# Optimization experiments

Measured on AMD Instinct MI355X. Metric: run time of the kernel, lower is better.

## Reference

```python
import jax, jax.numpy as jnp
import numpy as np

N_NODES = 100000
N_EDGES = 1600000
IN_CH = 128
HID = 128
NUM_CLASSES = 10
NUM_GRAPHS = 128
SLOPE = 0.01  # F.leaky_relu default negative_slope


def _lin_params(key, fan_in, fan_out):
    kw, kb = jax.random.split(key)
    bound = 1.0 / np.sqrt(fan_in)
    W = jax.random.uniform(kw, (fan_in, fan_out), jnp.float32, -bound, bound)
    b = jax.random.uniform(kb, (fan_out,), jnp.float32, -bound, bound)
    return W, b


def setup_inputs() -> dict:
    key = jax.random.key(0)
    ks = jax.random.split(key, 8)
    x = jax.random.normal(ks[0], (N_NODES, IN_CH), jnp.float32)
    edge_index = jax.random.randint(ks[1], (2, N_EDGES), 0, N_NODES, jnp.int64)
    batch = jnp.sort(jax.random.randint(ks[2], (N_NODES,), 0, NUM_GRAPHS, jnp.int64))
    W1, b1 = _lin_params(ks[3], IN_CH, HID)
    W2, b2 = _lin_params(ks[4], HID, HID)
    W3, b3 = _lin_params(ks[5], HID, HID // 2)
    W4, b4 = _lin_params(ks[6], HID // 2, HID // 2)
    W5, b5 = _lin_params(ks[7], HID // 2, NUM_CLASSES)
    return {"x": x, "edge_index": edge_index, "batch": batch,
            "W1": W1, "b1": b1, "W2": W2, "b2": b2,
            "W3": W3, "b3": b3, "W4": W4, "b4": b4, "W5": W5, "b5": b5}


def gcn_conv(x, src, dst, W, b):
    # PyG GCNConv: h = x W; add self-loops; symmetric norm D^-1/2 (A+I) D^-1/2
    h = x @ W  # [N, F]
    n = x.shape[0]
    deg = jnp.zeros((n,), h.dtype).at[dst].add(1.0) + 1.0  # includes self-loop
    dinv = jax.lax.rsqrt(deg)
    norm = dinv[src] * dinv[dst]  # [E]
    agg = jnp.zeros_like(h).at[dst].add(h[src] * norm[:, None])
    agg = agg + h * (dinv * dinv)[:, None]  # self-loop term: 1/deg
    return agg + b


def reference(x, edge_index, batch, W1, b1, W2, b2, W3, b3, W4, b4, W5, b5):
    src, dst = edge_index[0], edge_index[1]
    h = jax.nn.leaky_relu(gcn_conv(x, src, dst, W1, b1), SLOPE)
    h = jax.nn.leaky_relu(gcn_conv(h, src, dst, W2, b2), SLOPE)
    # global mean pool over graphs
    sums = jax.ops.segment_sum(h, batch, num_segments=NUM_GRAPHS)
    cnts = jax.ops.segment_sum(jnp.ones((h.shape[0],), h.dtype), batch,
                               num_segments=NUM_GRAPHS)
    g = sums / jnp.maximum(cnts, 1.0)[:, None]  # [NUM_GRAPHS, HID]
    g = jax.nn.leaky_relu(g @ W3 + b3, SLOPE)
    g = jax.nn.leaky_relu(g @ W4 + b4, SLOPE)
    return g @ W5 + b5
```

## Files before the change

kernel.cpp:

```cpp
#include <hip/hip_runtime.h>
#include <hip/hip_bf16.h>


#define SLOPE 0.01f

__device__ __forceinline__ float lrelu(float x) { return x > 0.f ? x : SLOPE * x; }

__device__ __forceinline__ unsigned short f2bf(float f) {
    union { float f; unsigned u; } v; v.f = f;
    unsigned r = v.u + 0x7fffu + ((v.u >> 16) & 1u);
    return (unsigned short)(r >> 16);
}
__device__ __forceinline__ float bf2f(unsigned short h) {
    union { unsigned u; float f; } v; v.u = ((unsigned)h) << 16;
    return v.f;
}
__device__ __forceinline__ float bf_lo(unsigned x) {
    union { unsigned u; float f; } v; v.u = x << 16; return v.f;
}
__device__ __forceinline__ float bf_hi(unsigned x) {
    union { unsigned u; float f; } v; v.u = x & 0xffff0000u; return v.f;
}
__device__ __forceinline__ unsigned packbf(float lo, float hi) {
    return (unsigned)f2bf(lo) | ((unsigned)f2bf(hi) << 16);
}

typedef __attribute__((ext_vector_type(8))) short bf16x8;
typedef __attribute__((ext_vector_type(4))) float f32x4;
typedef __attribute__((ext_vector_type(2))) float f32x2;

#define LDA 136
#define CAPP 5120
#define MAXBUCK 400

__global__ void k_init(int* __restrict__ zbase, int nz,
                       const float* __restrict__ W1, unsigned short* __restrict__ WT1,
                       const float* __restrict__ W2, unsigned short* __restrict__ WT2) {
    int b = blockIdx.x;
    if (b < 64) {
        int idx = b * 256 + threadIdx.x;
        int k = idx >> 7, n = idx & 127;
        WT1[n * 128 + k] = f2bf(W1[idx]);
    } else if (b < 128) {
        int idx = (b - 64) * 256 + threadIdx.x;
        int k = idx >> 7, n = idx & 127;
        WT2[n * 128 + k] = f2bf(W2[idx]);
    } else {
        int i = (b - 128) * 256 + threadIdx.x;
        if (i < nz) zbase[i] = 0;
    }
}

template<bool IN_BF16, bool SCALE>
__device__ __forceinline__ void gemm_body(const void* __restrict__ Xv,
                                          const unsigned short* __restrict__ WT,
                                          unsigned short* __restrict__ Y, int M,
                                          unsigned short* Bs, int bid,
                                          const float* __restrict__ dinvg) {
    int t = threadIdx.x;
    int row0 = bid * 64;
    int w = t >> 6, l = t & 63;
    int lr = l & 15;
    int ko = (l >> 4) * 8;

    int gr = row0 + w * 16 + lr;
    bool inb = gr < M;
    bf16x8 afr[4];
    if (IN_BF16) {
        const unsigned short* Xrow = (const unsigned short*)Xv + (size_t)gr * 128;
#pragma unroll
        for (int kc = 0; kc < 4; ++kc) {
            if (inb) afr[kc] = *(const bf16x8*)&Xrow[kc * 32 + ko];
            else     afr[kc] = (bf16x8){0, 0, 0, 0, 0, 0, 0, 0};
        }
    } else {
        const float* Xrow = (const float*)Xv + (size_t)gr * 128;
#pragma unroll
        for (int kc = 0; kc < 4; ++kc) {
            if (inb) {
                float4 u0 = *(const float4*)&Xrow[kc * 32 + ko];
                float4 u1 = *(const float4*)&Xrow[kc * 32 + ko + 4];
                union { bf16x8 v; unsigned u[4]; } cv;
                cv.u[0] = packbf(u0.x, u0.y);
                cv.u[1] = packbf(u0.z, u0.w);
                cv.u[2] = packbf(u1.x, u1.y);
                cv.u[3] = packbf(u1.z, u1.w);
                afr[kc] = cv.v;
            } else afr[kc] = (bf16x8){0, 0, 0, 0, 0, 0, 0, 0};
        }
    }

    {
        const uint4* WT4 = (const uint4*)WT;
#pragma unroll
        for (int i = 0; i < 8; ++i) {
            int idx = t + i * 256;
            int n = idx >> 4, c8 = idx & 15;
            *(uint4*)&Bs[n * LDA + c8 * 8] = WT4[idx];
        }
    }
    __syncthreads();

    f32x4 acc[8];
#pragma unroll
    for (int c = 0; c < 8; ++c) acc[c] = (f32x4){0.f, 0.f, 0.f, 0.f};

#pragma unroll
    for (int kc = 0; kc < 4; ++kc) {
        int kb = kc * 32 + ko;
        bf16x8 bfr[8];
#pragma unroll
        for (int ct = 0; ct < 8; ++ct)
            bfr[ct] = *(const bf16x8*)&Bs[(ct * 16 + lr) * LDA + kb];
#pragma unroll
        for (int ct = 0; ct < 8; ++ct)
            acc[ct] = __builtin_amdgcn_mfma_f32_16x16x32_bf16(afr[kc], bfr[ct], acc[ct], 0, 0, 0);
    }

    __syncthreads();
    int qr = (l >> 4) * 4;
#pragma unroll
    for (int i = 0; i < 4; ++i) {
        int r = w * 16 + qr + i;
        float sc = 1.f;
        if (SCALE) {
            int gr2 = row0 + r;
            sc = (gr2 < M) ? dinvg[gr2] : 1.f;
        }
#pragma unroll
        for (int ct = 0; ct < 8; ++ct)
            Bs[r * LDA + ct * 16 + lr] = f2bf(acc[ct][i] * sc);
    }
    __syncthreads();
    {
        uint4* Y4 = (uint4*)Y;
#pragma unroll
        for (int i = 0; i < 4; ++i) {
            int idx = t + i * 256;
            int r = idx >> 4, c8 = idx & 15;
            int g2 = row0 + r;
            if (g2 < M) Y4[(size_t)g2 * 16 + c8] = *(const uint4*)&Bs[r * LDA + c8 * 8];
        }
    }
}

__device__ __forceinline__ void p1_body(const int* __restrict__ src,
                                        const int* __restrict__ dst,
                                        int E, int nb, int* __restrict__ g_cnt,
                                        unsigned* __restrict__ part,
                                        int* hist, int bid) {
    int* base = hist + MAXBUCK;
    int t = threadIdx.x;
    for (int b = t; b < nb; b += 256) hist[b] = 0;
    __syncthreads();
    int e0b = bid * 4096;
#pragma unroll
    for (int j = 0; j < 4; ++j) {
        int e = e0b + j * 1024 + t * 4;
        if (e + 3 < E) {
            int4 d = *(const int4*)&dst[e];
            atomicAdd(&hist[d.x >> 8], 1);
            atomicAdd(&hist[d.y >> 8], 1);
            atomicAdd(&hist[d.z >> 8], 1);
            atomicAdd(&hist[d.w >> 8], 1);
        } else {
            for (int k = e; k < E && k < e + 4; ++k)
                atomicAdd(&hist[dst[k] >> 8], 1);
        }
    }
    __syncthreads();
    for (int b = t; b < nb; b += 256) {
        int c = hist[b];
        base[b] = c ? atomicAdd(&g_cnt[b], c) : 0;
        hist[b] = 0;
    }
    __syncthreads();
#pragma unroll
    for (int j = 0; j < 4; ++j) {
        int e = e0b + j * 1024 + t * 4;
        if (e + 3 < E) {
            int4 d = *(const int4*)&dst[e];
            int4 s = *(const int4*)&src[e];
            int bk, p;
            bk = d.x >> 8; p = base[bk] + atomicAdd(&hist[bk], 1);
            if (p < CAPP) part[(size_t)bk * CAPP + p] = ((unsigned)s.x << 8) | ((unsigned)d.x & 255u);
            bk = d.y >> 8; p = base[bk] + atomicAdd(&hist[bk], 1);
            if (p < CAPP) part[(size_t)bk * CAPP + p] = ((unsigned)s.y << 8) | ((unsigned)d.y & 255u);
            bk = d.z >> 8; p = base[bk] + atomicAdd(&hist[bk], 1);
            if (p < CAPP) part[(size_t)bk * CAPP + p] = ((unsigned)s.z << 8) | ((unsigned)d.z & 255u);
            bk = d.w >> 8; p = base[bk] + atomicAdd(&hist[bk], 1);
            if (p < CAPP) part[(size_t)bk * CAPP + p] = ((unsigned)s.w << 8) | ((unsigned)d.w & 255u);
        } else {
            for (int k = e; k < E && k < e + 4; ++k) {
                int bk = dst[k] >> 8;
                int p = base[bk] + atomicAdd(&hist[bk], 1);
                if (p < CAPP) part[(size_t)bk * CAPP + p] = ((unsigned)src[k] << 8) | ((unsigned)dst[k] & 255u);
            }
        }
    }
}

__global__ __launch_bounds__(256) void k_p1_gemm1(
    const int* __restrict__ src, const int* __restrict__ dst, int E, int nb,
    int* __restrict__ g_cnt, unsigned* __restrict__ part, int nbP1,
    const float* __restrict__ X, const unsigned short* __restrict__ WT,
    unsigned short* __restrict__ Y, int M) {
    __shared__ __align__(16) unsigned short Bs[128 * LDA];
    int b = blockIdx.x;
    if (b < nbP1) p1_body(src, dst, E, nb, g_cnt, part, (int*)Bs, b);
    else gemm_body<false, false>((const void*)X, WT, Y, M, Bs, b - nbP1, nullptr);
}

__global__ __launch_bounds__(256) void k_p2(const unsigned* __restrict__ part,
                                            const int* __restrict__ g_cnt,
                                            int* __restrict__ csr,
                                            int2* __restrict__ rpz,
                                            float* __restrict__ dinvg,
                                            unsigned short* __restrict__ H, int N) {
    __shared__ int cnt[256];
    __shared__ int sc[256];
    __shared__ float dvl[256];
    int b = blockIdx.x, t = threadIdx.x;
    int nbase = b << 8;
    int nn = N - nbase; if (nn > 256) nn = 256;

    cnt[t] = 0;
    __syncthreads();

    int Eb = g_cnt[b]; if (Eb > CAPP) Eb = CAPP;
    const unsigned* pp = part + (size_t)b * CAPP;
    for (int i = t; i < Eb; i += 256)
        atomicAdd(&cnt[pp[i] & 255u], 1);
    __syncthreads();

    int v = cnt[t];
    sc[t] = v;
    __syncthreads();
    for (int off = 1; off < 256; off <<= 1) {
        int add = (t >= off) ? sc[t - off] : 0;
        __syncthreads();
        sc[t] += add;
        __syncthreads();
    }
    int excl = sc[t] - v;

    float di = rsqrtf((float)v + 1.0f);
    if (t < nn) {
        rpz[nbase + t] = make_int2(b * CAPP + excl, b * CAPP + excl + v);
        dinvg[nbase + t] = di;
    }
    dvl[t] = di;
    cnt[t] = excl;
    __syncthreads();

    for (int i = t; i < Eb; i += 256) {
        unsigned pv = pp[i];
        int lcl = pv & 255u;
        int p = atomicAdd(&cnt[lcl], 1);
        csr[(size_t)b * CAPP + p] = (int)(pv >> 8);
    }

    uint4* H4 = (uint4*)H;
    int tot = nn * 16;
    for (int i = t; i < tot; i += 256) {
        int r = i >> 4, c = i & 15;
        float d = dvl[r];
        uint4 hv = H4[(size_t)(nbase + r) * 16 + c];
        uint4 o;
        o.x = packbf(bf_lo(hv.x) * d, bf_hi(hv.x) * d);
        o.y = packbf(bf_lo(hv.y) * d, bf_hi(hv.y) * d);
        o.z = packbf(bf_lo(hv.z) * d, bf_hi(hv.z) * d);
        o.w = packbf(bf_lo(hv.w) * d, bf_hi(hv.w) * d);
        H4[(size_t)(nbase + r) * 16 + c] = o;
    }
}

__global__ __launch_bounds__(256) void k_gemm2(
    const void* __restrict__ Xv, const unsigned short* __restrict__ WT,
    unsigned short* __restrict__ Y, int M, const float* __restrict__ dinvg) {
    __shared__ __align__(16) unsigned short Bs[128 * LDA];
    gemm_body<true, true>(Xv, WT, Y, M, Bs, blockIdx.x, dinvg);
}

__device__ __forceinline__ void acc8(f32x2& S0, f32x2& S1, f32x2& S2, f32x2& S3,
                                     uint4 hv) {
    f32x2 t;
    t.x = bf_lo(hv.x); t.y = bf_hi(hv.x); S0 += t;
    t.x = bf_lo(hv.y); t.y = bf_hi(hv.y); S1 += t;
    t.x = bf_lo(hv.z); t.y = bf_hi(hv.z); S2 += t;
    t.x = bf_lo(hv.w); t.y = bf_hi(hv.w); S3 += t;
}

__global__ __launch_bounds__(256) void k_agg7(const unsigned short* __restrict__ H,
                                              const int* __restrict__ csr,
                                              const int2* __restrict__ rpz,
                                              const float* __restrict__ dinvg,
                                              const float* __restrict__ bias,
                                              unsigned short* __restrict__ OUT, int N) {
    int t = threadIdx.x;
    int grp = t >> 4, cl = t & 15;
    int u = blockIdx.x * 16 + grp;
    if (u >= N) return;
    const uint4* H4 = (const uint4*)H;

    int2 rz = rpz[u];
    int e0 = rz.x, e1 = rz.y;
    uint4 hs = H4[(size_t)u * 16 + cl];
    float du = dinvg[u];

    f32x2 A0 = {0.f, 0.f}, A1 = {0.f, 0.f}, A2 = {0.f, 0.f}, A3 = {0.f, 0.f};
    f32x2 B0 = {0.f, 0.f}, B1 = {0.f, 0.f}, B2 = {0.f, 0.f}, B3 = {0.f, 0.f};

    int e = e0;
    while (e < e1) {
        int nn = e1 - e; if (nn > 16) nn = 16;
        int ci = (cl < nn) ? csr[e + cl] : 0;
        int j = 0;
        for (; j + 4 <= nn; j += 4) {
            int i0 = __shfl(ci, j,     16);
            int i1 = __shfl(ci, j + 1, 16);
            int i2 = __shfl(ci, j + 2, 16);
            int i3 = __shfl(ci, j + 3, 16);
            uint4 hA = H4[(size_t)i0 * 16 + cl];
            uint4 hB = H4[(size_t)i1 * 16 + cl];
            uint4 hC = H4[(size_t)i2 * 16 + cl];
            uint4 hD = H4[(size_t)i3 * 16 + cl];
            acc8(A0, A1, A2, A3, hA);
            acc8(B0, B1, B2, B3, hB);
            acc8(A0, A1, A2, A3, hC);
            acc8(B0, B1, B2, B3, hD);
        }
        for (; j < nn; ++j) {
            int i0 = __shfl(ci, j, 16);
            uint4 hA = H4[(size_t)i0 * 16 + cl];
            acc8(A0, A1, A2, A3, hA);
        }
        e += nn;
    }

    acc8(A0, A1, A2, A3, hs);
    A0 += B0; A1 += B1; A2 += B2; A3 += B3;
    float a0 = A0.x, a1 = A0.y, a2 = A1.x, a3 = A1.y;
    float a4 = A2.x, a5 = A2.y, a6 = A3.x, a7 = A3.y;

    float4 c0 = *(const float4*)&bias[cl * 8];
    float4 c1 = *(const float4*)&bias[cl * 8 + 4];
    uint4 o;
    o.x = packbf(lrelu(a0 * du + c0.x), lrelu(a1 * du + c0.y));
    o.y = packbf(lrelu(a2 * du + c0.z), lrelu(a3 * du + c0.w));
    o.z = packbf(lrelu(a4 * du + c1.x), lrelu(a5 * du + c1.y));
    o.w = packbf(lrelu(a6 * du + c1.z), lrelu(a7 * du + c1.w));
    ((uint4*)OUT)[(size_t)u * 16 + cl] = o;
}

#define PCH 128
__global__ __launch_bounds__(256) void k_pool3(const unsigned short* __restrict__ H,
                                               const int* __restrict__ batch,
                                               float* __restrict__ Gsum,
                                               int* __restrict__ Gcnt, int N) {
    int t = threadIdx.x;
    int st = t >> 6, c2 = t & 63;
    int n0 = blockIdx.x * PCH + st * (PCH / 4);
    int n1 = n0 + (PCH / 4); if (n1 > N) n1 = N;
    if (n0 >= N) return;
    float a0 = 0.f, a1 = 0.f;
    int cur = batch[n0], runstart = n0;
    for (int n = n0; n < n1; ++n) {
        int g = batch[n];
        if (g != cur) {
            atomicAdd(&Gsum[cur * 128 + c2 * 2], a0);
            atomicAdd(&Gsum[cur * 128 + c2 * 2 + 1], a1);
            if (c2 == 0) atomicAdd(&Gcnt[cur], n - runstart);
            a0 = a1 = 0.f; cur = g; runstart = n;
        }
        unsigned hv = *(const unsigned*)&H[(size_t)n * 128 + c2 * 2];
        a0 += bf_lo(hv); a1 += bf_hi(hv);
    }
    atomicAdd(&Gsum[cur * 128 + c2 * 2], a0);
    atomicAdd(&Gsum[cur * 128 + c2 * 2 + 1], a1);
    if (c2 == 0) atomicAdd(&Gcnt[cur], n1 - runstart);
}

__global__ __launch_bounds__(64) void k_mlp(const float* __restrict__ Gsum,
                                            const int* __restrict__ Gcnt,
                                            const float* __restrict__ W3, const float* __restrict__ b3,
                                            const float* __restrict__ W4, const float* __restrict__ b4,
                                            const float* __restrict__ W5, const float* __restrict__ b5,
                                            float* __restrict__ OUT) {
    __shared__ float row[128];
    __shared__ float t1[64];
    __shared__ float t2[64];
    int g = blockIdx.x, t = threadIdx.x;
    float inv = 1.0f / fmaxf((float)Gcnt[g], 1.0f);
    row[t]      = Gsum[g * 128 + t] * inv;
    row[t + 64] = Gsum[g * 128 + t + 64] * inv;
    __syncthreads();
    float acc = b3[t];
    for (int k = 0; k < 128; ++k) acc += row[k] * W3[k * 64 + t];
    t1[t] = lrelu(acc);
    __syncthreads();
    acc = b4[t];
    for (int k = 0; k < 64; ++k) acc += t1[k] * W4[k * 64 + t];
    t2[t] = lrelu(acc);
    __syncthreads();
    if (t < 10) {
        acc = b5[t];
        for (int k = 0; k < 64; ++k) acc += t2[k] * W5[k * 10 + t];
        OUT[g * 10 + t] = acc;
    }
}


extern "C" void kernel_launch(void* const* d_in, const int* in_sizes, int n_in,
                              void* d_out, int out_size, void* d_ws, size_t ws_size,
                              hipStream_t stream) {
    const float* x    = (const float*)d_in[0];
    const int*   ei   = (const int*)d_in[1];
    const int*   batch= (const int*)d_in[2];
    const float* W1   = (const float*)d_in[3];
    const float* b1   = (const float*)d_in[4];
    const float* W2   = (const float*)d_in[5];
    const float* b2   = (const float*)d_in[6];
    const float* W3   = (const float*)d_in[7];
    const float* b3   = (const float*)d_in[8];
    const float* W4   = (const float*)d_in[9];
    const float* b4   = (const float*)d_in[10];
    const float* W5   = (const float*)d_in[11];
    const float* b5   = (const float*)d_in[12];
    float* out = (float*)d_out;

    const int N = in_sizes[2];
    const int E = in_sizes[1] / 2;
    const int NG = 128;

    const int* src = ei;
    const int* dst = ei + E;

    char* w = (char*)d_ws;
    unsigned short* bufA = (unsigned short*)w; w += (size_t)N * 128 * 2;
    unsigned short* bufB = (unsigned short*)w; w += (size_t)N * 128 * 2;
    int*   g_cnt = (int*)w;   w += 512 * 4;
    float* gsum  = (float*)w; w += (size_t)NG * 128 * 4;
    int*   gcnt  = (int*)w;   w += (size_t)NG * 4;
    float* dinv  = (float*)w; w += (size_t)N * 4;
    int2*  rpz   = (int2*)w;  w += (size_t)N * 8;
    unsigned* part = (unsigned*)w; w += (size_t)MAXBUCK * CAPP * 4;
    int*   csr   = (int*)w;   w += (size_t)MAXBUCK * CAPP * 4;
    unsigned short* WT1 = (unsigned short*)w; w += 128 * 128 * 2;
    unsigned short* WT2 = (unsigned short*)w; w += 128 * 128 * 2;
    (void)ws_size; (void)n_in; (void)out_size;

    int nbB  = (N + 255) >> 8;
    int nbP1 = (E + 4095) / 4096;
    int nbG  = (N + 63) / 64;
    int nZero = 512 + NG * 128 + NG;
    int nbZ  = (nZero + 255) / 256;

    k_init<<<128 + nbZ, 256, 0, stream>>>(g_cnt, nZero, W1, WT1, W2, WT2);
    k_p1_gemm1<<<nbP1 + nbG, 256, 0, stream>>>(src, dst, E, nbB, g_cnt, part,
                                               nbP1, x, WT1, bufA, N);
    k_p2<<<nbB, 256, 0, stream>>>(part, g_cnt, csr, rpz, dinv, bufA, N);

    int nbA = (N + 15) / 16;

    k_agg7<<<nbA, 256, 0, stream>>>(bufA, csr, rpz, dinv, b1, bufB, N);
    k_gemm2<<<nbG, 256, 0, stream>>>(bufB, WT2, bufA, N, dinv);
    k_agg7<<<nbA, 256, 0, stream>>>(bufA, csr, rpz, dinv, b2, bufB, N);

    int nbP = (N + PCH - 1) / PCH;
    k_pool3<<<nbP, 256, 0, stream>>>(bufB, batch, gsum, gcnt, N);
    k_mlp<<<NG, 64, 0, stream>>>(gsum, gcnt, W3, b3, W4, b4, W5, b5, out);
}
```

Baseline: 332.4 us.

## Use nontemporal loads/stores and per-graph segment pooling via binary-searched starts

Streaming global loads and stores in the edge partition, GEMM, aggregation and pooling kernels become nontemporal, so single-use data is meant to pollute the caches less. Pooling becomes one block per graph. Segment starts come from a binary search over the sorted batch array, computed in the init kernel. This replaces atomic run-length accumulation and removes the need to zero gsum and gcnt. The cost is that pooling now runs on only 128 blocks, which may underuse the GPU, and nontemporal hints could hurt reuse of H rows that aggregation gathers again.

```diff
diff --git a/kernel.cpp b/kernel.cpp
--- a/kernel.cpp
+++ b/kernel.cpp
@@ -11,10 +11,6 @@
     unsigned r = v.u + 0x7fffu + ((v.u >> 16) & 1u);
     return (unsigned short)(r >> 16);
 }
-__device__ __forceinline__ float bf2f(unsigned short h) {
-    union { unsigned u; float f; } v; v.u = ((unsigned)h) << 16;
-    return v.f;
-}
 __device__ __forceinline__ float bf_lo(unsigned x) {
     union { unsigned u; float f; } v; v.u = x << 16; return v.f;
 }
@@ -28,6 +24,30 @@
 typedef __attribute__((ext_vector_type(8))) short bf16x8;
 typedef __attribute__((ext_vector_type(4))) float f32x4;
 typedef __attribute__((ext_vector_type(2))) float f32x2;
+typedef __attribute__((ext_vector_type(4))) unsigned u32x4;
+typedef __attribute__((ext_vector_type(4))) int i32x4;
+typedef __attribute__((ext_vector_type(2))) int i32x2;
+
+__device__ __forceinline__ uint4 nt_load_u4(const void* p) {
+    u32x4 v = __builtin_nontemporal_load((const u32x4*)p);
+    return make_uint4(v.x, v.y, v.z, v.w);
+}
+__device__ __forceinline__ void nt_store_u4(void* p, uint4 q) {
+    u32x4 v = {q.x, q.y, q.z, q.w};
+    __builtin_nontemporal_store(v, (u32x4*)p);
+}
+__device__ __forceinline__ int4 nt_load_i4(const void* p) {
+    i32x4 v = __builtin_nontemporal_load((const i32x4*)p);
+    return make_int4(v.x, v.y, v.z, v.w);
+}
+__device__ __forceinline__ int2 nt_load_i2(const void* p) {
+    i32x2 v = __builtin_nontemporal_load((const i32x2*)p);
+    return make_int2(v.x, v.y);
+}
+__device__ __forceinline__ float4 nt_load_f4(const void* p) {
+    f32x4 v = __builtin_nontemporal_load((const f32x4*)p);
+    return make_float4(v.x, v.y, v.z, v.w);
+}
 
 #define LDA 136
 #define CAPP 5120
@@ -35,7 +55,9 @@
 
 __global__ void k_init(int* __restrict__ zbase, int nz,
                        const float* __restrict__ W1, unsigned short* __restrict__ WT1,
-                       const float* __restrict__ W2, unsigned short* __restrict__ WT2) {
+                       const float* __restrict__ W2, unsigned short* __restrict__ WT2,
+                       const int* __restrict__ batch, int* __restrict__ gstart,
+                       int N, int NG) {
     int b = blockIdx.x;
     if (b < 64) {
         int idx = b * 256 + threadIdx.x;
@@ -45,8 +67,15 @@
         int idx = (b - 64) * 256 + threadIdx.x;
         int k = idx >> 7, n = idx & 127;
         WT2[n * 128 + k] = f2bf(W2[idx]);
+    } else if (b == 128) {
+        int g = threadIdx.x;
+        if (g <= NG) {
+            int lo = 0, hi = N;
+            while (lo < hi) { int mid = (lo + hi) >> 1; if (batch[mid] < g) lo = mid + 1; else hi = mid; }
+            gstart[g] = lo;
+        }
     } else {
-        int i = (b - 128) * 256 + threadIdx.x;
+        int i = (b - 129) * 256 + threadIdx.x;
         if (i < nz) zbase[i] = 0;
     }
 }
@@ -70,7 +99,7 @@
         const unsigned short* Xrow = (const unsigned short*)Xv + (size_t)gr * 128;
 #pragma unroll
         for (int kc = 0; kc < 4; ++kc) {
-            if (inb) afr[kc] = *(const bf16x8*)&Xrow[kc * 32 + ko];
+            if (inb) afr[kc] = __builtin_nontemporal_load((const bf16x8*)&Xrow[kc * 32 + ko]);
             else     afr[kc] = (bf16x8){0, 0, 0, 0, 0, 0, 0, 0};
         }
     } else {
@@ -78,8 +107,8 @@
 #pragma unroll
         for (int kc = 0; kc < 4; ++kc) {
             if (inb) {
-                float4 u0 = *(const float4*)&Xrow[kc * 32 + ko];
-                float4 u1 = *(const float4*)&Xrow[kc * 32 + ko + 4];
+                float4 u0 = nt_load_f4(&Xrow[kc * 32 + ko]);
+                float4 u1 = nt_load_f4(&Xrow[kc * 32 + ko + 4]);
                 union { bf16x8 v; unsigned u[4]; } cv;
                 cv.u[0] = packbf(u0.x, u0.y);
                 cv.u[1] = packbf(u0.z, u0.w);
@@ -139,7 +168,7 @@
             int idx = t + i * 256;
             int r = idx >> 4, c8 = idx & 15;
             int g2 = row0 + r;
-            if (g2 < M) Y4[(size_t)g2 * 16 + c8] = *(const uint4*)&Bs[r * LDA + c8 * 8];
+            if (g2 < M) nt_store_u4(&Y4[(size_t)g2 * 16 + c8], *(const uint4*)&Bs[r * LDA + c8 * 8]);
         }
     }
 }
@@ -158,7 +187,7 @@
     for (int j = 0; j < 4; ++j) {
         int e = e0b + j * 1024 + t * 4;
         if (e + 3 < E) {
-            int4 d = *(const int4*)&dst[e];
+            int4 d = nt_load_i4(&dst[e]);
             atomicAdd(&hist[d.x >> 8], 1);
             atomicAdd(&hist[d.y >> 8], 1);
             atomicAdd(&hist[d.z >> 8], 1);
@@ -179,17 +208,17 @@
     for (int j = 0; j < 4; ++j) {
         int e = e0b + j * 1024 + t * 4;
         if (e + 3 < E) {
-            int4 d = *(const int4*)&dst[e];
-            int4 s = *(const int4*)&src[e];
+            int4 d = nt_load_i4(&dst[e]);
+            int4 s = nt_load_i4(&src[e]);
             int bk, p;
             bk = d.x >> 8; p = base[bk] + atomicAdd(&hist[bk], 1);
-            if (p < CAPP) part[(size_t)bk * CAPP + p] = ((unsigned)s.x << 8) | ((unsigned)d.x & 255u);
+            if (p < CAPP) __builtin_nontemporal_store(((unsigned)s.x << 8) | ((unsigned)d.x & 255u), &part[(size_t)bk * CAPP + p]);
             bk = d.y >> 8; p = base[bk] + atomicAdd(&hist[bk], 1);
-            if (p < CAPP) part[(size_t)bk * CAPP + p] = ((unsigned)s.y << 8) | ((unsigned)d.y & 255u);
+            if (p < CAPP) __builtin_nontemporal_store(((unsigned)s.y << 8) | ((unsigned)d.y & 255u), &part[(size_t)bk * CAPP + p]);
             bk = d.z >> 8; p = base[bk] + atomicAdd(&hist[bk], 1);
-            if (p < CAPP) part[(size_t)bk * CAPP + p] = ((unsigned)s.z << 8) | ((unsigned)d.z & 255u);
+            if (p < CAPP) __builtin_nontemporal_store(((unsigned)s.z << 8) | ((unsigned)d.z & 255u), &part[(size_t)bk * CAPP + p]);
             bk = d.w >> 8; p = base[bk] + atomicAdd(&hist[bk], 1);
-            if (p < CAPP) part[(size_t)bk * CAPP + p] = ((unsigned)s.w << 8) | ((unsigned)d.w & 255u);
+            if (p < CAPP) __builtin_nontemporal_store(((unsigned)s.w << 8) | ((unsigned)d.w & 255u), &part[(size_t)bk * CAPP + p]);
         } else {
             for (int k = e; k < E && k < e + 4; ++k) {
                 int bk = dst[k] >> 8;
@@ -230,7 +259,7 @@
     int Eb = g_cnt[b]; if (Eb > CAPP) Eb = CAPP;
     const unsigned* pp = part + (size_t)b * CAPP;
     for (int i = t; i < Eb; i += 256)
-        atomicAdd(&cnt[pp[i] & 255u], 1);
+        atomicAdd(&cnt[__builtin_nontemporal_load(&pp[i]) & 255u], 1);
     __syncthreads();
 
     int v = cnt[t];
@@ -254,10 +283,10 @@
     __syncthreads();
 
     for (int i = t; i < Eb; i += 256) {
-        unsigned pv = pp[i];
+        unsigned pv = __builtin_nontemporal_load(&pp[i]);
         int lcl = pv & 255u;
         int p = atomicAdd(&cnt[lcl], 1);
-        csr[(size_t)b * CAPP + p] = (int)(pv >> 8);
+        __builtin_nontemporal_store((int)(pv >> 8), &csr[(size_t)b * CAPP + p]);
     }
 
     uint4* H4 = (uint4*)H;
@@ -303,7 +332,7 @@
     if (u >= N) return;
     const uint4* H4 = (const uint4*)H;
 
-    int2 rz = rpz[u];
+    int2 rz = nt_load_i2(&rpz[u]);
     int e0 = rz.x, e1 = rz.y;
     uint4 hs = H4[(size_t)u * 16 + cl];
     float du = dinvg[u];
@@ -314,7 +343,7 @@
     int e = e0;
     while (e < e1) {
         int nn = e1 - e; if (nn > 16) nn = 16;
-        int ci = (cl < nn) ? csr[e + cl] : 0;
+        int ci = (cl < nn) ? __builtin_nontemporal_load(&csr[e + cl]) : 0;
         int j = 0;
         for (; j + 4 <= nn; j += 4) {
             int i0 = __shfl(ci, j,     16);
@@ -350,39 +379,29 @@
     o.y = packbf(lrelu(a2 * du + c0.z), lrelu(a3 * du + c0.w));
     o.z = packbf(lrelu(a4 * du + c1.x), lrelu(a5 * du + c1.y));
     o.w = packbf(lrelu(a6 * du + c1.z), lrelu(a7 * du + c1.w));
-    ((uint4*)OUT)[(size_t)u * 16 + cl] = o;
-}
-
-#define PCH 128
-__global__ __launch_bounds__(256) void k_pool3(const unsigned short* __restrict__ H,
-                                               const int* __restrict__ batch,
-                                               float* __restrict__ Gsum,
-                                               int* __restrict__ Gcnt, int N) {
-    int t = threadIdx.x;
+    nt_store_u4(&((uint4*)OUT)[(size_t)u * 16 + cl], o);
+}
+
+__global__ __launch_bounds__(256) void k_pool4(const unsigned short* __restrict__ H,
+                                               const int* __restrict__ gstart,
+                                               float* __restrict__ Gsum) {
+    __shared__ float red[4][128];
+    int g = blockIdx.x, t = threadIdx.x;
     int st = t >> 6, c2 = t & 63;
-    int n0 = blockIdx.x * PCH + st * (PCH / 4);
-    int n1 = n0 + (PCH / 4); if (n1 > N) n1 = N;
-    if (n0 >= N) return;
+    int gs = gstart[g], ge = gstart[g + 1];
     float a0 = 0.f, a1 = 0.f;
-    int cur = batch[n0], runstart = n0;
-    for (int n = n0; n < n1; ++n) {
-        int g = batch[n];
-        if (g != cur) {
-            atomicAdd(&Gsum[cur * 128 + c2 * 2], a0);
-            atomicAdd(&Gsum[cur * 128 + c2 * 2 + 1], a1);
-            if (c2 == 0) atomicAdd(&Gcnt[cur], n - runstart);
-            a0 = a1 = 0.f; cur = g; runstart = n;
-        }
-        unsigned hv = *(const unsigned*)&H[(size_t)n * 128 + c2 * 2];
+    for (int n = gs + st; n < ge; n += 4) {
+        unsigned hv = __builtin_nontemporal_load((const unsigned*)&H[(size_t)n * 128 + c2 * 2]);
         a0 += bf_lo(hv); a1 += bf_hi(hv);
     }
-    atomicAdd(&Gsum[cur * 128 + c2 * 2], a0);
-    atomicAdd(&Gsum[cur * 128 + c2 * 2 + 1], a1);
-    if (c2 == 0) atomicAdd(&Gcnt[cur], n1 - runstart);
+    red[st][c2 * 2] = a0; red[st][c2 * 2 + 1] = a1;
+    __syncthreads();
+    if (t < 128)
+        Gsum[g * 128 + t] = red[0][t] + red[1][t] + red[2][t] + red[3][t];
 }
 
 __global__ __launch_bounds__(64) void k_mlp(const float* __restrict__ Gsum,
-                                            const int* __restrict__ Gcnt,
+                                            const int* __restrict__ gstart,
                                             const float* __restrict__ W3, const float* __restrict__ b3,
                                             const float* __restrict__ W4, const float* __restrict__ b4,
                                             const float* __restrict__ W5, const float* __restrict__ b5,
@@ -391,7 +410,7 @@
     __shared__ float t1[64];
     __shared__ float t2[64];
     int g = blockIdx.x, t = threadIdx.x;
-    float inv = 1.0f / fmaxf((float)Gcnt[g], 1.0f);
+    float inv = 1.0f / fmaxf((float)(gstart[g + 1] - gstart[g]), 1.0f);
     row[t]      = Gsum[g * 128 + t] * inv;
     row[t + 64] = Gsum[g * 128 + t + 64] * inv;
     __syncthreads();
@@ -441,7 +460,7 @@
     unsigned short* bufB = (unsigned short*)w; w += (size_t)N * 128 * 2;
     int*   g_cnt = (int*)w;   w += 512 * 4;
     float* gsum  = (float*)w; w += (size_t)NG * 128 * 4;
-    int*   gcnt  = (int*)w;   w += (size_t)NG * 4;
+    int*   gstart= (int*)w;   w += 512 * 4;
     float* dinv  = (float*)w; w += (size_t)N * 4;
     int2*  rpz   = (int2*)w;  w += (size_t)N * 8;
     unsigned* part = (unsigned*)w; w += (size_t)MAXBUCK * CAPP * 4;
@@ -453,10 +472,11 @@
     int nbB  = (N + 255) >> 8;
     int nbP1 = (E + 4095) / 4096;
     int nbG  = (N + 63) / 64;
-    int nZero = 512 + NG * 128 + NG;
+    int nZero = 512;
     int nbZ  = (nZero + 255) / 256;
 
-    k_init<<<128 + nbZ, 256, 0, stream>>>(g_cnt, nZero, W1, WT1, W2, WT2);
+    k_init<<<129 + nbZ, 256, 0, stream>>>(g_cnt, nZero, W1, WT1, W2, WT2,
+                                          batch, gstart, N, NG);
     k_p1_gemm1<<<nbP1 + nbG, 256, 0, stream>>>(src, dst, E, nbB, g_cnt, part,
                                                nbP1, x, WT1, bufA, N);
     k_p2<<<nbB, 256, 0, stream>>>(part, g_cnt, csr, rpz, dinv, bufA, N);
@@ -467,7 +487,6 @@
     k_gemm2<<<nbG, 256, 0, stream>>>(bufB, WT2, bufA, N, dinv);
     k_agg7<<<nbA, 256, 0, stream>>>(bufA, csr, rpz, dinv, b2, bufB, N);
 
-    int nbP = (N + PCH - 1) / PCH;
-    k_pool3<<<nbP, 256, 0, stream>>>(bufB, batch, gsum, gcnt, N);
-    k_mlp<<<NG, 64, 0, stream>>>(gsum, gcnt, W3, b3, W4, b4, W5, b5, out);
-}
+    k_pool4<<<NG, 256, 0, stream>>>(bufB, gstart, gsum);
+    k_mlp<<<NG, 64, 0, stream>>>(gsum, gstart, W3, b3, W4, b4, W5, b5, out);
+}
```

New measurement: 469.8 us. +41.3%, slower.

## Slice node features into 8 channel-blocks so each aggregation block gathers a narrow slice

Applied to the files above, without the earlier changes.

Node feature buffers are stored as 8 slices of 16 channels ([slice][node][16]), and the aggregation kernel assigns one slice per block, with two threads per node handling 32 bytes each. The aim is to shrink the per-slice working set (N*32 bytes) so random neighbour gathers hit L2/cache better than 256-byte full-row gathers spread over the whole table. GEMM loads and stores, the dinv rescale, pooling and the MLP channel mapping are all rewritten for the new layout. Separately, per-graph node counts now come from a binary search over the sorted batch array instead of atomic counts in pooling. The cost is that each edge index is read 8 times and each gather uses narrower 32-byte segments.

```diff
diff --git a/kernel.cpp b/kernel.cpp
--- a/kernel.cpp
+++ b/kernel.cpp
@@ -11,10 +11,6 @@
     unsigned r = v.u + 0x7fffu + ((v.u >> 16) & 1u);
     return (unsigned short)(r >> 16);
 }
-__device__ __forceinline__ float bf2f(unsigned short h) {
-    union { unsigned u; float f; } v; v.u = ((unsigned)h) << 16;
-    return v.f;
-}
 __device__ __forceinline__ float bf_lo(unsigned x) {
     union { unsigned u; float f; } v; v.u = x << 16; return v.f;
 }
@@ -33,9 +29,12 @@
 #define CAPP 5120
 #define MAXBUCK 400
 
+
 __global__ void k_init(int* __restrict__ zbase, int nz,
                        const float* __restrict__ W1, unsigned short* __restrict__ WT1,
-                       const float* __restrict__ W2, unsigned short* __restrict__ WT2) {
+                       const float* __restrict__ W2, unsigned short* __restrict__ WT2,
+                       const int* __restrict__ batch, int* __restrict__ gstart,
+                       int N, int NG) {
     int b = blockIdx.x;
     if (b < 64) {
         int idx = b * 256 + threadIdx.x;
@@ -45,8 +44,15 @@
         int idx = (b - 64) * 256 + threadIdx.x;
         int k = idx >> 7, n = idx & 127;
         WT2[n * 128 + k] = f2bf(W2[idx]);
+    } else if (b == 128) {
+        int g = threadIdx.x;
+        if (g <= NG) {
+            int lo = 0, hi = N;
+            while (lo < hi) { int mid = (lo + hi) >> 1; if (batch[mid] < g) lo = mid + 1; else hi = mid; }
+            gstart[g] = lo;
+        }
     } else {
-        int i = (b - 128) * 256 + threadIdx.x;
+        int i = (b - 129) * 256 + threadIdx.x;
         if (i < nz) zbase[i] = 0;
     }
 }
@@ -67,10 +73,11 @@
     bool inb = gr < M;
     bf16x8 afr[4];
     if (IN_BF16) {
-        const unsigned short* Xrow = (const unsigned short*)Xv + (size_t)gr * 128;
+        const unsigned short* Hsb = (const unsigned short*)Xv;
 #pragma unroll
         for (int kc = 0; kc < 4; ++kc) {
-            if (inb) afr[kc] = *(const bf16x8*)&Xrow[kc * 32 + ko];
+            int c0 = kc * 32 + ko;
+            if (inb) afr[kc] = *(const bf16x8*)&Hsb[((size_t)(c0 >> 4) * M + gr) * 16 + (c0 & 15)];
             else     afr[kc] = (bf16x8){0, 0, 0, 0, 0, 0, 0, 0};
         }
     } else {
@@ -139,7 +146,8 @@
             int idx = t + i * 256;
             int r = idx >> 4, c8 = idx & 15;
             int g2 = row0 + r;
-            if (g2 < M) Y4[(size_t)g2 * 16 + c8] = *(const uint4*)&Bs[r * LDA + c8 * 8];
+            if (g2 < M)
+                Y4[((size_t)(c8 >> 1) * M + g2) * 2 + (c8 & 1)] = *(const uint4*)&Bs[r * LDA + c8 * 8];
         }
     }
 }
@@ -263,15 +271,16 @@
     uint4* H4 = (uint4*)H;
     int tot = nn * 16;
     for (int i = t; i < tot; i += 256) {
-        int r = i >> 4, c = i & 15;
+        int r = i >> 4, q = i & 15;
         float d = dvl[r];
-        uint4 hv = H4[(size_t)(nbase + r) * 16 + c];
+        size_t idx = ((size_t)(q >> 1) * N + nbase + r) * 2 + (q & 1);
+        uint4 hv = H4[idx];
         uint4 o;
         o.x = packbf(bf_lo(hv.x) * d, bf_hi(hv.x) * d);
         o.y = packbf(bf_lo(hv.y) * d, bf_hi(hv.y) * d);
         o.z = packbf(bf_lo(hv.z) * d, bf_hi(hv.z) * d);
         o.w = packbf(bf_lo(hv.w) * d, bf_hi(hv.w) * d);
-        H4[(size_t)(nbase + r) * 16 + c] = o;
+        H4[idx] = o;
     }
 }
 
@@ -291,78 +300,76 @@
     t.x = bf_lo(hv.w); t.y = bf_hi(hv.w); S3 += t;
 }
 
-__global__ __launch_bounds__(256) void k_agg7(const unsigned short* __restrict__ H,
+__global__ __launch_bounds__(256) void k_agg8(const unsigned short* __restrict__ Hs,
                                               const int* __restrict__ csr,
                                               const int2* __restrict__ rpz,
                                               const float* __restrict__ dinvg,
                                               const float* __restrict__ bias,
-                                              unsigned short* __restrict__ OUT, int N) {
+                                              unsigned short* __restrict__ OUTs, int N) {
+    int b = blockIdx.x;
+    int s = b & 7;
+    int nb = b >> 3;
     int t = threadIdx.x;
-    int grp = t >> 4, cl = t & 15;
-    int u = blockIdx.x * 16 + grp;
+    int pair = t >> 1, half = t & 1;
+    int u = nb * 128 + pair;
     if (u >= N) return;
-    const uint4* H4 = (const uint4*)H;
+    const uint4* H4 = (const uint4*)Hs + (size_t)s * N * 2;
 
     int2 rz = rpz[u];
-    int e0 = rz.x, e1 = rz.y;
-    uint4 hs = H4[(size_t)u * 16 + cl];
     float du = dinvg[u];
+    uint4 hsv = H4[(size_t)u * 2 + half];
 
     f32x2 A0 = {0.f, 0.f}, A1 = {0.f, 0.f}, A2 = {0.f, 0.f}, A3 = {0.f, 0.f};
     f32x2 B0 = {0.f, 0.f}, B1 = {0.f, 0.f}, B2 = {0.f, 0.f}, B3 = {0.f, 0.f};
-
-    int e = e0;
+    const uint4 z4 = make_uint4(0, 0, 0, 0);
+
+    int e = rz.x, e1 = rz.y;
     while (e < e1) {
-        int nn = e1 - e; if (nn > 16) nn = 16;
-        int ci = (cl < nn) ? csr[e + cl] : 0;
-        int j = 0;
-        for (; j + 4 <= nn; j += 4) {
-            int i0 = __shfl(ci, j,     16);
-            int i1 = __shfl(ci, j + 1, 16);
-            int i2 = __shfl(ci, j + 2, 16);
-            int i3 = __shfl(ci, j + 3, 16);
-            uint4 hA = H4[(size_t)i0 * 16 + cl];
-            uint4 hB = H4[(size_t)i1 * 16 + cl];
-            uint4 hC = H4[(size_t)i2 * 16 + cl];
-            uint4 hD = H4[(size_t)i3 * 16 + cl];
-            acc8(A0, A1, A2, A3, hA);
-            acc8(B0, B1, B2, B3, hB);
-            acc8(A0, A1, A2, A3, hC);
-            acc8(B0, B1, B2, B3, hD);
-        }
-        for (; j < nn; ++j) {
-            int i0 = __shfl(ci, j, 16);
-            uint4 hA = H4[(size_t)i0 * 16 + cl];
-            acc8(A0, A1, A2, A3, hA);
-        }
+        int nn = e1 - e; if (nn > 4) nn = 4;
+        int cA = (e + half < e1)     ? csr[e + half]     : 0;
+        int cB = (e + 2 + half < e1) ? csr[e + 2 + half] : 0;
+        int i0 = __shfl(cA, 0, 2);
+        int i1 = __shfl(cA, 1, 2);
+        int i2 = __shfl(cB, 0, 2);
+        int i3 = __shfl(cB, 1, 2);
+        uint4 h0 =            H4[(size_t)i0 * 2 + half];
+        uint4 h1 = (nn > 1) ? H4[(size_t)i1 * 2 + half] : z4;
+        uint4 h2 = (nn > 2) ? H4[(size_t)i2 * 2 + half] : z4;
+        uint4 h3 = (nn > 3) ? H4[(size_t)i3 * 2 + half] : z4;
+        acc8(A0, A1, A2, A3, h0);
+        acc8(B0, B1, B2, B3, h1);
+        acc8(A0, A1, A2, A3, h2);
+        acc8(B0, B1, B2, B3, h3);
         e += nn;
     }
 
-    acc8(A0, A1, A2, A3, hs);
     A0 += B0; A1 += B1; A2 += B2; A3 += B3;
+    acc8(A0, A1, A2, A3, hsv);
     float a0 = A0.x, a1 = A0.y, a2 = A1.x, a3 = A1.y;
     float a4 = A2.x, a5 = A2.y, a6 = A3.x, a7 = A3.y;
 
-    float4 c0 = *(const float4*)&bias[cl * 8];
-    float4 c1 = *(const float4*)&bias[cl * 8 + 4];
+    const float* bs = bias + s * 16 + half * 8;
+    float4 c0 = *(const float4*)bs;
+    float4 c1 = *(const float4*)(bs + 4);
     uint4 o;
     o.x = packbf(lrelu(a0 * du + c0.x), lrelu(a1 * du + c0.y));
     o.y = packbf(lrelu(a2 * du + c0.z), lrelu(a3 * du + c0.w));
     o.z = packbf(lrelu(a4 * du + c1.x), lrelu(a5 * du + c1.y));
     o.w = packbf(lrelu(a6 * du + c1.z), lrelu(a7 * du + c1.w));
-    ((uint4*)OUT)[(size_t)u * 16 + cl] = o;
+    ((uint4*)OUTs)[((size_t)s * N + u) * 2 + half] = o;
 }
 
 #define PCH 128
-__global__ __launch_bounds__(256) void k_pool3(const unsigned short* __restrict__ H,
+__global__ __launch_bounds__(256) void k_pool5(const unsigned short* __restrict__ H,
                                                const int* __restrict__ batch,
-                                               float* __restrict__ Gsum,
-                                               int* __restrict__ Gcnt, int N) {
+                                               float* __restrict__ Gsum, int N) {
     int t = threadIdx.x;
     int st = t >> 6, c2 = t & 63;
     int n0 = blockIdx.x * PCH + st * (PCH / 4);
     int n1 = n0 + (PCH / 4); if (n1 > N) n1 = N;
     if (n0 >= N) return;
+    size_t sb = (size_t)(c2 >> 3) * N;
+    int off = (c2 & 7) * 2;
     float a0 = 0.f, a1 = 0.f;
     int cur = batch[n0], runstart = n0;
     for (int n = n0; n < n1; ++n) {
@@ -370,19 +377,18 @@
         if (g != cur) {
             atomicAdd(&Gsum[cur * 128 + c2 * 2], a0);
             atomicAdd(&Gsum[cur * 128 + c2 * 2 + 1], a1);
-            if (c2 == 0) atomicAdd(&Gcnt[cur], n - runstart);
             a0 = a1 = 0.f; cur = g; runstart = n;
         }
-        unsigned hv = *(const unsigned*)&H[(size_t)n * 128 + c2 * 2];
+        unsigned hv = *(const unsigned*)&H[(sb + n) * 16 + off];
         a0 += bf_lo(hv); a1 += bf_hi(hv);
     }
     atomicAdd(&Gsum[cur * 128 + c2 * 2], a0);
     atomicAdd(&Gsum[cur * 128 + c2 * 2 + 1], a1);
-    if (c2 == 0) atomicAdd(&Gcnt[cur], n1 - runstart);
+    (void)runstart;
 }
 
 __global__ __launch_bounds__(64) void k_mlp(const float* __restrict__ Gsum,
-                                            const int* __restrict__ Gcnt,
+                                            const int* __restrict__ gstart,
                                             const float* __restrict__ W3, const float* __restrict__ b3,
                                             const float* __restrict__ W4, const float* __restrict__ b4,
                                             const float* __restrict__ W5, const float* __restrict__ b5,
@@ -391,9 +397,13 @@
     __shared__ float t1[64];
     __shared__ float t2[64];
     int g = blockIdx.x, t = threadIdx.x;
-    float inv = 1.0f / fmaxf((float)Gcnt[g], 1.0f);
-    row[t]      = Gsum[g * 128 + t] * inv;
-    row[t + 64] = Gsum[g * 128 + t + 64] * inv;
+    float inv = 1.0f / fmaxf((float)(gstart[g + 1] - gstart[g]), 1.0f);
+    int c2 = t >> 1, lohi = t & 1;
+    int gch = ((c2 >> 3) << 4) + ((c2 & 7) << 1) + lohi;
+    row[gch] = Gsum[g * 128 + t] * inv;
+    c2 = (t + 64) >> 1; lohi = (t + 64) & 1;
+    gch = ((c2 >> 3) << 4) + ((c2 & 7) << 1) + lohi;
+    row[gch] = Gsum[g * 128 + t + 64] * inv;
     __syncthreads();
     float acc = b3[t];
     for (int k = 0; k < 128; ++k) acc += row[k] * W3[k * 64 + t];
@@ -441,7 +451,7 @@
     unsigned short* bufB = (unsigned short*)w; w += (size_t)N * 128 * 2;
     int*   g_cnt = (int*)w;   w += 512 * 4;
     float* gsum  = (float*)w; w += (size_t)NG * 128 * 4;
-    int*   gcnt  = (int*)w;   w += (size_t)NG * 4;
+    int*   gstart= (int*)w;   w += 512 * 4;
     float* dinv  = (float*)w; w += (size_t)N * 4;
     int2*  rpz   = (int2*)w;  w += (size_t)N * 8;
     unsigned* part = (unsigned*)w; w += (size_t)MAXBUCK * CAPP * 4;
@@ -453,21 +463,22 @@
     int nbB  = (N + 255) >> 8;
     int nbP1 = (E + 4095) / 4096;
     int nbG  = (N + 63) / 64;
-    int nZero = 512 + NG * 128 + NG;
+    int nZero = 512 + NG * 128;
     int nbZ  = (nZero + 255) / 256;
 
-    k_init<<<128 + nbZ, 256, 0, stream>>>(g_cnt, nZero, W1, WT1, W2, WT2);
+    k_init<<<129 + nbZ, 256, 0, stream>>>(g_cnt, nZero, W1, WT1, W2, WT2,
+                                          batch, gstart, N, NG);
     k_p1_gemm1<<<nbP1 + nbG, 256, 0, stream>>>(src, dst, E, nbB, g_cnt, part,
                                                nbP1, x, WT1, bufA, N);
     k_p2<<<nbB, 256, 0, stream>>>(part, g_cnt, csr, rpz, dinv, bufA, N);
 
-    int nbA = (N + 15) / 16;
-
-    k_agg7<<<nbA, 256, 0, stream>>>(bufA, csr, rpz, dinv, b1, bufB, N);
+    int nbA = ((N + 127) / 128) * 8;
+
+    k_agg8<<<nbA, 256, 0, stream>>>(bufA, csr, rpz, dinv, b1, bufB, N);
     k_gemm2<<<nbG, 256, 0, stream>>>(bufB, WT2, bufA, N, dinv);
-    k_agg7<<<nbA, 256, 0, stream>>>(bufA, csr, rpz, dinv, b2, bufB, N);
+    k_agg8<<<nbA, 256, 0, stream>>>(bufA, csr, rpz, dinv, b2, bufB, N);
 
     int nbP = (N + PCH - 1) / PCH;
-    k_pool3<<<nbP, 256, 0, stream>>>(bufB, batch, gsum, gcnt, N);
-    k_mlp<<<NG, 64, 0, stream>>>(gsum, gcnt, W3, b3, W4, b4, W5, b5, out);
-}
+    k_pool5<<<nbP, 256, 0, stream>>>(bufB, batch, gsum, N);
+    k_mlp<<<NG, 64, 0, stream>>>(gsum, gstart, W3, b3, W4, b4, W5, b5, out);
+}
```

Result: slower. 498.2 us (+49.9%).

## Fuse layer-1 aggregation with layer-2 GEMM and derive graph counts via binary search

Applied to the files above, without the earlier changes.

Layer-1 neighbor aggregation is now computed straight into shared memory and fed to the MFMA GEMM for layer 2 in the same kernel, so the intermediate activation no longer makes a global-memory round trip and one launch is removed. Per-graph node counts are now derived once from a binary search over the sorted batch array in the init kernel, which removes the count atomics from the pooling kernel. The fused kernel handles 64 rows per block, so there are fewer, heavier blocks for the gather phase, and the B operand is read straight from global memory rather than staged in LDS. The count shortcut depends on batch being sorted.

```diff
diff --git a/kernel.cpp b/kernel.cpp
--- a/kernel.cpp
+++ b/kernel.cpp
@@ -11,10 +11,6 @@
     unsigned r = v.u + 0x7fffu + ((v.u >> 16) & 1u);
     return (unsigned short)(r >> 16);
 }
-__device__ __forceinline__ float bf2f(unsigned short h) {
-    union { unsigned u; float f; } v; v.u = ((unsigned)h) << 16;
-    return v.f;
-}
 __device__ __forceinline__ float bf_lo(unsigned x) {
     union { unsigned u; float f; } v; v.u = x << 16; return v.f;
 }
@@ -35,7 +31,9 @@
 
 __global__ void k_init(int* __restrict__ zbase, int nz,
                        const float* __restrict__ W1, unsigned short* __restrict__ WT1,
-                       const float* __restrict__ W2, unsigned short* __restrict__ WT2) {
+                       const float* __restrict__ W2, unsigned short* __restrict__ WT2,
+                       const int* __restrict__ batch, int* __restrict__ gstart,
+                       int N, int NG) {
     int b = blockIdx.x;
     if (b < 64) {
         int idx = b * 256 + threadIdx.x;
@@ -45,8 +43,15 @@
         int idx = (b - 64) * 256 + threadIdx.x;
         int k = idx >> 7, n = idx & 127;
         WT2[n * 128 + k] = f2bf(W2[idx]);
+    } else if (b == 128) {
+        int g = threadIdx.x;
+        if (g <= NG) {
+            int lo = 0, hi = N;
+            while (lo < hi) { int mid = (lo + hi) >> 1; if (batch[mid] < g) lo = mid + 1; else hi = mid; }
+            gstart[g] = lo;
+        }
     } else {
-        int i = (b - 128) * 256 + threadIdx.x;
+        int i = (b - 129) * 256 + threadIdx.x;
         if (i < nz) zbase[i] = 0;
     }
 }
@@ -275,13 +280,6 @@
     }
 }
 
-__global__ __launch_bounds__(256) void k_gemm2(
-    const void* __restrict__ Xv, const unsigned short* __restrict__ WT,
-    unsigned short* __restrict__ Y, int M, const float* __restrict__ dinvg) {
-    __shared__ __align__(16) unsigned short Bs[128 * LDA];
-    gemm_body<true, true>(Xv, WT, Y, M, Bs, blockIdx.x, dinvg);
-}
-
 __device__ __forceinline__ void acc8(f32x2& S0, f32x2& S1, f32x2& S2, f32x2& S3,
                                      uint4 hv) {
     f32x2 t;
@@ -291,23 +289,11 @@
     t.x = bf_lo(hv.w); t.y = bf_hi(hv.w); S3 += t;
 }
 
-__global__ __launch_bounds__(256) void k_agg7(const unsigned short* __restrict__ H,
-                                              const int* __restrict__ csr,
-                                              const int2* __restrict__ rpz,
-                                              const float* __restrict__ dinvg,
-                                              const float* __restrict__ bias,
-                                              unsigned short* __restrict__ OUT, int N) {
-    int t = threadIdx.x;
-    int grp = t >> 4, cl = t & 15;
-    int u = blockIdx.x * 16 + grp;
-    if (u >= N) return;
-    const uint4* H4 = (const uint4*)H;
-
-    int2 rz = rpz[u];
-    int e0 = rz.x, e1 = rz.y;
+__device__ __forceinline__ uint4 agg_node(const uint4* __restrict__ H4,
+                                          const int* __restrict__ csr,
+                                          int e0, int e1, int u, float du,
+                                          const float* __restrict__ bias, int cl) {
     uint4 hs = H4[(size_t)u * 16 + cl];
-    float du = dinvg[u];
-
     f32x2 A0 = {0.f, 0.f}, A1 = {0.f, 0.f}, A2 = {0.f, 0.f}, A3 = {0.f, 0.f};
     f32x2 B0 = {0.f, 0.f}, B1 = {0.f, 0.f}, B2 = {0.f, 0.f}, B3 = {0.f, 0.f};
 
@@ -350,39 +336,124 @@
     o.y = packbf(lrelu(a2 * du + c0.z), lrelu(a3 * du + c0.w));
     o.z = packbf(lrelu(a4 * du + c1.x), lrelu(a5 * du + c1.y));
     o.w = packbf(lrelu(a6 * du + c1.z), lrelu(a7 * du + c1.w));
+    return o;
+}
+
+__global__ __launch_bounds__(256) void k_aggemm(
+    const unsigned short* __restrict__ H,
+    const int* __restrict__ csr, const int2* __restrict__ rpz,
+    const float* __restrict__ dinvg, const float* __restrict__ bias,
+    const unsigned short* __restrict__ WT,
+    unsigned short* __restrict__ Y, int M) {
+    __shared__ __align__(16) unsigned short As[64 * LDA];
+    int t = threadIdx.x;
+    int row0 = blockIdx.x * 64;
+    int grp = t >> 4, cl = t & 15;
+    const uint4* H4 = (const uint4*)H;
+
+#pragma unroll
+    for (int rd = 0; rd < 4; ++rd) {
+        int r = rd * 16 + grp;
+        int u = row0 + r;
+        uint4 o = make_uint4(0, 0, 0, 0);
+        if (u < M) {
+            int2 rz = rpz[u];
+            float du = dinvg[u];
+            o = agg_node(H4, csr, rz.x, rz.y, u, du, bias, cl);
+        }
+        *(uint4*)&As[r * LDA + cl * 8] = o;
+    }
+    __syncthreads();
+
+    int w = t >> 6, l = t & 63;
+    int lr = l & 15;
+    int ko = (l >> 4) * 8;
+
+    f32x4 acc[8];
+#pragma unroll
+    for (int c = 0; c < 8; ++c) acc[c] = (f32x4){0.f, 0.f, 0.f, 0.f};
+
+#pragma unroll
+    for (int kc = 0; kc < 4; ++kc) {
+        int kb = kc * 32 + ko;
+        bf16x8 afr = *(const bf16x8*)&As[(w * 16 + lr) * LDA + kb];
+        bf16x8 bfr[8];
+#pragma unroll
+        for (int ct = 0; ct < 8; ++ct)
+            bfr[ct] = *(const bf16x8*)&WT[(size_t)(ct * 16 + lr) * 128 + kb];
+#pragma unroll
+        for (int ct = 0; ct < 8; ++ct)
+            acc[ct] = __builtin_amdgcn_mfma_f32_16x16x32_bf16(afr, bfr[ct], acc[ct], 0, 0, 0);
+    }
+
+    __syncthreads();
+    int qr = (l >> 4) * 4;
+#pragma unroll
+    for (int i = 0; i < 4; ++i) {
+        int r = w * 16 + qr + i;
+        int gr2 = row0 + r;
+        float sc = (gr2 < M) ? dinvg[gr2] : 1.f;
+#pragma unroll
+        for (int ct = 0; ct < 8; ++ct)
+            As[r * LDA + ct * 16 + lr] = f2bf(acc[ct][i] * sc);
+    }
+    __syncthreads();
+    {
+        uint4* Y4 = (uint4*)Y;
+#pragma unroll
+        for (int i = 0; i < 4; ++i) {
+            int idx = t + i * 256;
+            int r = idx >> 4, c8 = idx & 15;
+            int g2 = row0 + r;
+            if (g2 < M) Y4[(size_t)g2 * 16 + c8] = *(const uint4*)&As[r * LDA + c8 * 8];
+        }
+    }
+}
+
+__global__ __launch_bounds__(256) void k_agg7(const unsigned short* __restrict__ H,
+                                              const int* __restrict__ csr,
+                                              const int2* __restrict__ rpz,
+                                              const float* __restrict__ dinvg,
+                                              const float* __restrict__ bias,
+                                              unsigned short* __restrict__ OUT, int N) {
+    int t = threadIdx.x;
+    int grp = t >> 4, cl = t & 15;
+    int u = blockIdx.x * 16 + grp;
+    if (u >= N) return;
+    const uint4* H4 = (const uint4*)H;
+    int2 rz = rpz[u];
+    float du = dinvg[u];
+    uint4 o = agg_node(H4, csr, rz.x, rz.y, u, du, bias, cl);
     ((uint4*)OUT)[(size_t)u * 16 + cl] = o;
 }
 
 #define PCH 128
 __global__ __launch_bounds__(256) void k_pool3(const unsigned short* __restrict__ H,
                                                const int* __restrict__ batch,
-                                               float* __restrict__ Gsum,
-                                               int* __restrict__ Gcnt, int N) {
+                                               float* __restrict__ Gsum, int N) {
     int t = threadIdx.x;
     int st = t >> 6, c2 = t & 63;
     int n0 = blockIdx.x * PCH + st * (PCH / 4);
     int n1 = n0 + (PCH / 4); if (n1 > N) n1 = N;
     if (n0 >= N) return;
     float a0 = 0.f, a1 = 0.f;
-    int cur = batch[n0], runstart = n0;
+    int cur = batch[n0];
     for (int n = n0; n < n1; ++n) {
         int g = batch[n];
         if (g != cur) {
             atomicAdd(&Gsum[cur * 128 + c2 * 2], a0);
             atomicAdd(&Gsum[cur * 128 + c2 * 2 + 1], a1);
-            if (c2 == 0) atomicAdd(&Gcnt[cur], n - runstart);
-            a0 = a1 = 0.f; cur = g; runstart = n;
+            a0 = a1 = 0.f; cur = g;
         }
         unsigned hv = *(const unsigned*)&H[(size_t)n * 128 + c2 * 2];
         a0 += bf_lo(hv); a1 += bf_hi(hv);
     }
     atomicAdd(&Gsum[cur * 128 + c2 * 2], a0);
     atomicAdd(&Gsum[cur * 128 + c2 * 2 + 1], a1);
-    if (c2 == 0) atomicAdd(&Gcnt[cur], n1 - runstart);
 }
 
 __global__ __launch_bounds__(64) void k_mlp(const float* __restrict__ Gsum,
-                                            const int* __restrict__ Gcnt,
+                                            const int* __restrict__ gstart,
                                             const float* __restrict__ W3, const float* __restrict__ b3,
                                             const float* __restrict__ W4, const float* __restrict__ b4,
                                             const float* __restrict__ W5, const float* __restrict__ b5,
@@ -391,7 +462,7 @@
     __shared__ float t1[64];
     __shared__ float t2[64];
     int g = blockIdx.x, t = threadIdx.x;
-    float inv = 1.0f / fmaxf((float)Gcnt[g], 1.0f);
+    float inv = 1.0f / fmaxf((float)(gstart[g + 1] - gstart[g]), 1.0f);
     row[t]      = Gsum[g * 128 + t] * inv;
     row[t + 64] = Gsum[g * 128 + t + 64] * inv;
     __syncthreads();
@@ -441,7 +512,7 @@
     unsigned short* bufB = (unsigned short*)w; w += (size_t)N * 128 * 2;
     int*   g_cnt = (int*)w;   w += 512 * 4;
     float* gsum  = (float*)w; w += (size_t)NG * 128 * 4;
-    int*   gcnt  = (int*)w;   w += (size_t)NG * 4;
+    int*   gstart= (int*)w;   w += 512 * 4;
     float* dinv  = (float*)w; w += (size_t)N * 4;
     int2*  rpz   = (int2*)w;  w += (size_t)N * 8;
     unsigned* part = (unsigned*)w; w += (size_t)MAXBUCK * CAPP * 4;
@@ -453,21 +524,21 @@
     int nbB  = (N + 255) >> 8;
     int nbP1 = (E + 4095) / 4096;
     int nbG  = (N + 63) / 64;
-    int nZero = 512 + NG * 128 + NG;
+    int nZero = 512 + NG * 128;
     int nbZ  = (nZero + 255) / 256;
 
-    k_init<<<128 + nbZ, 256, 0, stream>>>(g_cnt, nZero, W1, WT1, W2, WT2);
+    k_init<<<129 + nbZ, 256, 0, stream>>>(g_cnt, nZero, W1, WT1, W2, WT2,
+                                          batch, gstart, N, NG);
     k_p1_gemm1<<<nbP1 + nbG, 256, 0, stream>>>(src, dst, E, nbB, g_cnt, part,
                                                nbP1, x, WT1, bufA, N);
     k_p2<<<nbB, 256, 0, stream>>>(part, g_cnt, csr, rpz, dinv, bufA, N);
 
+    k_aggemm<<<nbG, 256, 0, stream>>>(bufA, csr, rpz, dinv, b1, WT2, bufB, N);
+
     int nbA = (N + 15) / 16;
-
-    k_agg7<<<nbA, 256, 0, stream>>>(bufA, csr, rpz, dinv, b1, bufB, N);
-    k_gemm2<<<nbG, 256, 0, stream>>>(bufB, WT2, bufA, N, dinv);
-    k_agg7<<<nbA, 256, 0, stream>>>(bufA, csr, rpz, dinv, b2, bufB, N);
+    k_agg7<<<nbA, 256, 0, stream>>>(bufB, csr, rpz, dinv, b2, bufA, N);
 
     int nbP = (N + PCH - 1) / PCH;
-    k_pool3<<<nbP, 256, 0, stream>>>(bufB, batch, gsum, gcnt, N);
-    k_mlp<<<NG, 64, 0, stream>>>(gsum, gcnt, W3, b3, W4, b4, W5, b5, out);
-}
+    k_pool3<<<nbP, 256, 0, stream>>>(bufA, batch, gsum, N);
+    k_mlp<<<NG, 64, 0, stream>>>(gsum, gstart, W3, b3, W4, b4, W5, b5, out);
+}
```

After: 344.8 us. +3.7%, slower.
